# Kernel tuning notes

Measured on AMD Instinct MI355X. Metric: run time of the kernel, lower is better.

Reference implementation:

```python
import jax, jax.numpy as jnp
import numpy as np

EPS = 1e-6        # RMSNorm140 eps
LAM = 0.1         # lambda_: second-order score weight
HAD = 0.05        # hadamard_scale

def _rmsnorm(x, w):
    return x * jax.lax.rsqrt(jnp.mean(x * x, axis=-1, keepdims=True) + EPS) * w

def _rope(x):
    # x: [b, h, s, d]; interleaved-pair rotary embedding (theta=10000)
    b, h, s, d = x.shape
    inv = 1.0 / (10000.0 ** (jnp.arange(0, d, 2, dtype=jnp.float32) / d))
    ang = jnp.arange(s, dtype=jnp.float32)[:, None] * inv[None, :]  # [s, d/2]
    cos, sin = jnp.cos(ang), jnp.sin(ang)
    x1, x2 = x[..., 0::2], x[..., 1::2]
    out = jnp.stack([x1 * cos - x2 * sin, x1 * sin + x2 * cos], axis=-1)
    return out.reshape(b, h, s, d)

def _rotate_half(x):
    d = x.shape[-1] // 2
    return jnp.concatenate([-x[..., d:], x[..., :d]], axis=-1)

def _attn_pass(Q, K, V):
    # scores = (Q@K^T + lam * Q^2 @ (K^2)^T) / sqrt(head_dim)   (second-order amplify)
    scale = 1.0 / jnp.sqrt(jnp.float32(Q.shape[-1]))
    scores = (jnp.einsum('bhsd,bhtd->bhst', Q, K)
              + LAM * jnp.einsum('bhsd,bhtd->bhst', Q * Q, K * K)) * scale
    return jnp.einsum('bhst,bhtd->bhsd', jax.nn.softmax(scores, axis=-1), V)

def _attention(x, wq, wk, wv, wo, gate_w):
    b, s, dim = x.shape
    hd = gate_w.shape[0]
    nh = dim // hd
    def proj(w):  # StickyLinear: x @ W^T, W stored [out, in]
        return (x @ w.T).reshape(b, s, nh, hd).transpose(0, 2, 1, 3)  # [b,h,s,d]
    Q, K, V = proj(wq), proj(wk), proj(wv)
    Q, K = _rope(Q), _rope(K)
    out1 = _attn_pass(Q, K, V)
    # rotated second pass + per-channel sigmoid gate over head_dim
    out2 = _attn_pass(_rotate_half(Q), _rotate_half(K), V)
    g = jax.nn.sigmoid(gate_w)
    out = out1 * (1.0 - g) + out2 * g
    out = out + HAD * out * out  # Hadamard mix (elementwise nonlinearity)
    out = out.transpose(0, 2, 1, 3).reshape(b, s, dim)
    return out @ wo.T

def _ffn(x, w1, w3, w2):
    # SwiGLU: down( silu(gate(x)) * up(x) )
    return (jax.nn.silu(x @ w1.T) * (x @ w3.T)) @ w2.T

def reference(x, norm1_w, norm2_w, wq, wk, wv, wo, gate_w, w1, w3, w2):
    h = x + _attention(_rmsnorm(x, norm1_w), wq, wk, wv, wo, gate_w)
    return h + _ffn(_rmsnorm(h, norm2_w), w1, w3, w2)

def setup_inputs() -> dict:
    B, S, D, NH, DFF = 2, 1024, 2048, 16, 8192
    HD = D // NH
    key = jax.random.key(0)
    ks = jax.random.split(key, 9)
    std = 0.02
    return {
        'x': jax.random.normal(ks[0], (B, S, D), dtype=jnp.float32),
        'norm1_w': jnp.ones((D,), jnp.float32),
        'norm2_w': jnp.ones((D,), jnp.float32),
        'wq': jax.random.normal(ks[1], (D, D), jnp.float32) * std,
        'wk': jax.random.normal(ks[2], (D, D), jnp.float32) * std,
        'wv': jax.random.normal(ks[3], (D, D), jnp.float32) * std,
        'wo': jax.random.normal(ks[4], (D, D), jnp.float32) * std,
        'gate_w': jax.random.normal(ks[5], (HD,), jnp.float32) * 0.01,
        'w1': jax.random.normal(ks[6], (DFF, D), jnp.float32) * std,
        'w3': jax.random.normal(ks[7], (DFF, D), jnp.float32) * std,
        'w2': jax.random.normal(ks[8], (D, DFF), jnp.float32) * std,
    }
```

## Files before the change

kernel.cpp:

```cpp
#include <hip/hip_runtime.h>
#include <hip/hip_bf16.h>

typedef unsigned short u16;
typedef unsigned int u32;
typedef u16 u16x8 __attribute__((ext_vector_type(8)));
typedef float f32x4 __attribute__((ext_vector_type(4)));

__device__ __forceinline__ u16 f2bf(float f) {
  union { float f; u32 u; } v; v.f = f;
  u32 r = v.u + 0x7FFFu + ((v.u >> 16) & 1u);
  return (u16)(r >> 16);
}
__device__ __forceinline__ float bf2f(u16 h) {
  union { u32 u; float f; } v; v.u = ((u32)h) << 16;
  return v.f;
}
__device__ __forceinline__ void mfma_bf16_16x16x32(f32x4& acc, const f32x4& a, const f32x4& b) {
  asm("v_mfma_f32_16x16x32_bf16 %0, %1, %2, %0" : "+v"(acc) : "v"(a), "v"(b));
}
__device__ __forceinline__ void gload_lds16(const void* g, void* l) {
  __builtin_amdgcn_global_load_lds(
      (const __attribute__((address_space(1))) unsigned int*)g,
      (__attribute__((address_space(3))) unsigned int*)l, 16, 0, 0);
}

__global__ __launch_bounds__(256) void cvt_k(const float* __restrict__ src,
                                             u16* __restrict__ dst, int n8) {
  int i = blockIdx.x * 256 + threadIdx.x;
  if (i >= n8) return;
  float4 f0 = *(const float4*)&src[(size_t)i * 8];
  float4 f1 = *(const float4*)&src[(size_t)i * 8 + 4];
  u16x8 o;
  o[0] = f2bf(f0.x); o[1] = f2bf(f0.y); o[2] = f2bf(f0.z); o[3] = f2bf(f0.w);
  o[4] = f2bf(f1.x); o[5] = f2bf(f1.y); o[6] = f2bf(f1.z); o[7] = f2bf(f1.w);
  *(u16x8*)&dst[(size_t)i * 8] = o;
}

__global__ __launch_bounds__(256) void cvt13_k(const float* __restrict__ src,
                                               u16* __restrict__ dst, int half) {
  int r = blockIdx.x;
  int dr = ((r >> 4) << 5) + (r & 15) + (half << 4);
  int t = threadIdx.x;
  const float* s = src + (size_t)r * 2048 + t * 8;
  float4 f0 = *(const float4*)s;
  float4 f1 = *(const float4*)(s + 4);
  u16x8 o;
  o[0] = f2bf(f0.x); o[1] = f2bf(f0.y); o[2] = f2bf(f0.z); o[3] = f2bf(f0.w);
  o[4] = f2bf(f1.x); o[5] = f2bf(f1.y); o[6] = f2bf(f1.z); o[7] = f2bf(f1.w);
  *(u16x8*)&dst[(size_t)dr * 2048 + t * 8] = o;
}

__global__ __launch_bounds__(256) void rmsnorm_k(const float* __restrict__ X,
                                                 const float* __restrict__ W,
                                                 u16* __restrict__ O) {
  const int row = blockIdx.x;
  const int tid = threadIdx.x;
  const float* x = X + (size_t)row * 2048;
  float4 v0 = *(const float4*)&x[tid * 8];
  float4 v1 = *(const float4*)&x[tid * 8 + 4];
  float s = v0.x * v0.x + v0.y * v0.y + v0.z * v0.z + v0.w * v0.w
          + v1.x * v1.x + v1.y * v1.y + v1.z * v1.z + v1.w * v1.w;
  #pragma unroll
  for (int m = 1; m < 64; m <<= 1) s += __shfl_xor(s, m);
  __shared__ float red[4];
  if ((tid & 63) == 0) red[tid >> 6] = s;
  __syncthreads();
  float tot = red[0] + red[1] + red[2] + red[3];
  float r = rsqrtf(tot * (1.0f / 2048.0f) + 1e-6f);
  float4 w0 = *(const float4*)&W[tid * 8];
  float4 w1 = *(const float4*)&W[tid * 8 + 4];
  u16x8 o;
  o[0] = f2bf(v0.x * r * w0.x); o[1] = f2bf(v0.y * r * w0.y);
  o[2] = f2bf(v0.z * r * w0.z); o[3] = f2bf(v0.w * r * w0.w);
  o[4] = f2bf(v1.x * r * w1.x); o[5] = f2bf(v1.y * r * w1.y);
  o[6] = f2bf(v1.z * r * w1.z); o[7] = f2bf(v1.w * r * w1.w);
  *(u16x8*)&O[(size_t)row * 2048 + tid * 8] = o;
}

#define EPI_F32 0
#define EPI_ADDF32 1
#define EPI_SWIGLU 2

template <int EPI>
__global__ __launch_bounds__(256) void gemm_bt(const u16* __restrict__ A,
                                               const u16* __restrict__ B,
                                               float* __restrict__ Cf,
                                               u16* __restrict__ Cb,
                                               const float* __restrict__ R,
                                               int M, int N, int Kt,
                                               int lda, int ldb) {
  __shared__ __align__(16) u16 As[2][128 * 32];
  __shared__ __align__(16) u16 Bs[2][128 * 32];
  const int tid = threadIdx.x;
  const int lane = tid & 63;
  const int w = tid >> 6;
  const int wm = w >> 1, wn = w & 1;
  const int m0 = blockIdx.y * 128, n0 = blockIdx.x * 128;
  const int z = blockIdx.z;
  A += (size_t)z * Kt;
  B += (size_t)z * Kt;
  Cf += (size_t)z * M * N;
  const int r0 = tid >> 2;
  const int c0 = (tid & 3) * 8;
  const int r1 = r0 + 64;
  const int laneM = lane & 15;
  const int laneK = (lane >> 4) * 8;

  f32x4 acc[4][4];
  #pragma unroll
  for (int i = 0; i < 4; i++)
    #pragma unroll
    for (int j = 0; j < 4; j++) acc[i][j] = (f32x4){0.f, 0.f, 0.f, 0.f};

  const u16* Ar0 = &A[(size_t)(m0 + r0) * lda + c0];
  const u16* Ar1 = &A[(size_t)(m0 + r1) * lda + c0];
  const u16* Br0 = &B[(size_t)(n0 + r0) * ldb + c0];
  const u16* Br1 = &B[(size_t)(n0 + r1) * ldb + c0];
  const int lofs0 = r0 * 32 + c0;
  const int lofs1 = r1 * 32 + c0;

  auto stage = [&](int bsel, int kt) {
    gload_lds16(Ar0 + kt, &As[bsel][lofs0]);
    gload_lds16(Ar1 + kt, &As[bsel][lofs1]);
    gload_lds16(Br0 + kt, &Bs[bsel][lofs0]);
    gload_lds16(Br1 + kt, &Bs[bsel][lofs1]);
  };

  stage(0, 0);
  const int nt = Kt >> 5;
  for (int t = 0; t < nt; t++) {
    const int cur = t & 1;
    if (t + 1 < nt) {
      stage(cur ^ 1, (t + 1) << 5);
      asm volatile("s_waitcnt vmcnt(4)" ::: "memory");
    } else {
      asm volatile("s_waitcnt vmcnt(0)" ::: "memory");
    }
    __builtin_amdgcn_s_barrier();
    __builtin_amdgcn_sched_barrier(0);
    f32x4 af[4], bfr[4];
    #pragma unroll
    for (int mi = 0; mi < 4; mi++)
      af[mi] = *(const f32x4*)&As[cur][(wm * 64 + mi * 16 + laneM) * 32 + laneK];
    #pragma unroll
    for (int ni = 0; ni < 4; ni++)
      bfr[ni] = *(const f32x4*)&Bs[cur][(wn * 64 + ni * 16 + laneM) * 32 + laneK];
    #pragma unroll
    for (int mi = 0; mi < 4; mi++)
      #pragma unroll
      for (int ni = 0; ni < 4; ni++)
        mfma_bf16_16x16x32(acc[mi][ni], af[mi], bfr[ni]);
    __builtin_amdgcn_sched_barrier(0);
    __builtin_amdgcn_s_barrier();
  }

  const int rowb = (lane >> 4) * 4;
  const int coll = lane & 15;
  #pragma unroll
  for (int mi = 0; mi < 4; mi++) {
    #pragma unroll
    for (int i = 0; i < 4; i++) {
      int row = m0 + wm * 64 + mi * 16 + rowb + i;
      #pragma unroll
      for (int ni = 0; ni < 4; ni++) {
        int col = n0 + wn * 64 + ni * 16 + coll;
        size_t idx = (size_t)row * N + col;
        float v = acc[mi][ni][i];
        if constexpr (EPI == EPI_F32) Cf[idx] = v;
        else Cf[idx] = v + R[idx];
      }
    }
  }
}

template <int EPI>
__global__ __launch_bounds__(512, 2) void gemm256(const u16* __restrict__ A,
                                                  const u16* __restrict__ B,
                                                  float* __restrict__ Cf,
                                                  u16* __restrict__ Cb,
                                                  int M, int N, int Kt,
                                                  int lda, int ldb) {
  __shared__ __align__(16) char sm[131072];
  const int tid = threadIdx.x;
  const int lane = tid & 63, w = tid >> 6;
  const int wr = w >> 2, wc = w & 3;
  const int laneM = lane & 15, laneG = lane >> 4;
  const int m0 = blockIdx.y * 256, n0 = blockIdx.x * 256;
  const int z = blockIdx.z;
  A += (size_t)z * Kt;
  B += (size_t)z * Kt;
  Cf += (size_t)z * M * N;

  const int srow = tid >> 3;
  const int scb = (tid & 7) * 16;

  f32x4 acc[8][4];
  #pragma unroll
  for (int i = 0; i < 8; i++)
    #pragma unroll
    for (int j = 0; j < 4; j++) acc[i][j] = (f32x4){0.f, 0.f, 0.f, 0.f};

  auto stage = [&](int buf, int ktE, int ht) {
    const int half = ht & 1;
    const bool isA = ht < 2;
    char* base = sm + (isA ? 0 : 65536) + buf * 32768 + half * 16384;
    const u16* src = isA ? A : B;
    const int ld = isA ? lda : ldb;
    const int rb = (isA ? m0 : n0) + half * 128;
    #pragma unroll
    for (int j = 0; j < 2; j++) {
      int row = j * 64 + srow;
      int scol = (scb ^ ((row & 7) << 4)) >> 1;
      gload_lds16(src + (size_t)(rb + row) * ld + ktE + scol,
                  base + j * 8192 + tid * 16);
    }
  };

  const int nkt = Kt >> 6;
  #pragma unroll
  for (int ht = 0; ht < 4; ht++) stage(0, 0, ht);

  const int bHalf = wc >> 1;
  const int bRow0 = (wc & 1) * 64;

  for (int t = 0; t < nkt; t++) {
    const int cb_ = t & 1;
    char* aBase = sm + cb_ * 32768 + wr * 16384;
    char* bBase = sm + 65536 + cb_ * 32768 + bHalf * 16384;
    if (t + 1 < nkt) {
      #pragma unroll
      for (int ht = 0; ht < 4; ht++) stage(cb_ ^ 1, (t + 1) << 6, ht);
      asm volatile("s_waitcnt vmcnt(8)" ::: "memory");
    } else {
      asm volatile("s_waitcnt vmcnt(0)" ::: "memory");
    }
    __builtin_amdgcn_s_barrier();
    #pragma unroll
    for (int q = 0; q < 4; q++) {
      const int mh = q >> 1, nh = q & 1;
      f32x4 af[4][2], bg[2][2];
      #pragma unroll
      for (int mi = 0; mi < 4; mi++)
        #pragma unroll
        for (int ks = 0; ks < 2; ks++) {
          int r = (mh * 4 + mi) * 16 + laneM;
          int cbv = ks * 64 + laneG * 16;
          af[mi][ks] = *(const f32x4*)(aBase + r * 128 + (cbv ^ ((r & 7) << 4)));
        }
      #pragma unroll
      for (int ni = 0; ni < 2; ni++)
        #pragma unroll
        for (int ks = 0; ks < 2; ks++) {
          int r = bRow0 + (nh * 2 + ni) * 16 + laneM;
          int cbv = ks * 64 + laneG * 16;
          bg[ni][ks] = *(const f32x4*)(bBase + r * 128 + (cbv ^ ((r & 7) << 4)));
        }
      if (q > 0) __builtin_amdgcn_s_barrier();
      asm volatile("s_waitcnt lgkmcnt(0)" ::: "memory");
      __builtin_amdgcn_sched_barrier(0);
      __builtin_amdgcn_s_setprio(1);
      #pragma unroll
      for (int mi = 0; mi < 4; mi++)
        #pragma unroll
        for (int ni = 0; ni < 2; ni++)
          #pragma unroll
          for (int ks = 0; ks < 2; ks++)
            mfma_bf16_16x16x32(acc[mh * 4 + mi][nh * 2 + ni], af[mi][ks], bg[ni][ks]);
      __builtin_amdgcn_s_setprio(0);
      __builtin_amdgcn_sched_barrier(0);
      __builtin_amdgcn_s_barrier();
    }
  }

  #pragma unroll
  for (int mi = 0; mi < 8; mi++) {
    #pragma unroll
    for (int i = 0; i < 4; i++) {
      int row = m0 + wr * 128 + mi * 16 + laneG * 4 + i;
      if constexpr (EPI == EPI_SWIGLU) {
        #pragma unroll
        for (int np = 0; np < 2; np++) {
          float g = acc[mi][np * 2][i];
          float u = acc[mi][np * 2 + 1][i];
          float sg = g / (1.0f + __expf(-g));
          int j = (n0 >> 1) + wc * 32 + np * 16 + laneM;
          Cb[(size_t)row * (N >> 1) + j] = f2bf(sg * u);
        }
      } else {
        #pragma unroll
        for (int ni = 0; ni < 4; ni++) {
          int col = n0 + wc * 64 + ni * 16 + laneM;
          Cf[(size_t)row * N + col] = acc[mi][ni][i];
        }
      }
    }
  }
}

__global__ __launch_bounds__(256) void reduce5_k(const float* __restrict__ P,
                                                 const float* __restrict__ H,
                                                 float* __restrict__ out) {
  size_t i = ((size_t)blockIdx.x * 256 + threadIdx.x) * 4;
  const size_t MN = 4194304;
  float4 a = *(const float4*)&P[i];
  float4 b = *(const float4*)&P[MN + i];
  float4 c = *(const float4*)&P[2 * MN + i];
  float4 d = *(const float4*)&P[3 * MN + i];
  float4 h = *(const float4*)&H[i];
  float4 o;
  o.x = a.x + b.x + c.x + d.x + h.x;
  o.y = a.y + b.y + c.y + d.y + h.y;
  o.z = a.z + b.z + c.z + d.z + h.z;
  o.w = a.w + b.w + c.w + d.w + h.w;
  *(float4*)&out[i] = o;
}

__device__ __forceinline__ void rope_row(const float* __restrict__ src,
                                         u16* __restrict__ dst, int s, int q4) {
  float vv[32];
  #pragma unroll
  for (int t = 0; t < 8; t++) {
    float4 f = *(const float4*)&src[t * 4];
    vv[t * 4] = f.x; vv[t * 4 + 1] = f.y; vv[t * 4 + 2] = f.z; vv[t * 4 + 3] = f.w;
  }
  u16 o1[32], o2[32];
  #pragma unroll
  for (int jl = 0; jl < 16; jl++) {
    int j = q4 * 16 + jl;
    float inv = exp2f(-(float)j * 0.20762050593046014f);
    float ang = (float)s * inv;
    float sn, cs;
    __sincosf(ang, &sn, &cs);
    float a = vv[2 * jl], b = vv[2 * jl + 1];
    float r1 = a * cs - b * sn;
    float r2 = a * sn + b * cs;
    o1[2 * jl] = f2bf(r1);
    o1[2 * jl + 1] = f2bf(r2);
    o2[2 * jl] = f2bf(0.31622776601683794f * r1 * r1);
    o2[2 * jl + 1] = f2bf(0.31622776601683794f * r2 * r2);
  }
  #pragma unroll
  for (int t = 0; t < 4; t++) {
    *(u16x8*)&dst[q4 * 32 + t * 8] = *(const u16x8*)&o1[t * 8];
    *(u16x8*)&dst[128 + q4 * 32 + t * 8] = *(const u16x8*)&o2[t * 8];
  }
}

__global__ __launch_bounds__(256) void qkv_post_k(const float* __restrict__ QKVF,
                                                  u16* __restrict__ Qe,
                                                  u16* __restrict__ Ke,
                                                  u16* __restrict__ Vt) {
  const int st = blockIdx.x;
  const int bh = blockIdx.y;
  const int b = bh >> 4, h = bh & 15;
  const int tid = threadIdx.x;
  {
    int r = tid >> 2, q4 = tid & 3;
    int s = st * 64 + r;
    size_t rowin = ((size_t)b * 1024 + s) * 6144 + h * 128 + q4 * 32;
    size_t rowe = ((size_t)bh * 1024 + s) * 256;
    rope_row(QKVF + rowin, Qe + rowe, s, q4);
    rope_row(QKVF + rowin + 2048, Ke + rowe, s, q4);
  }
  __shared__ __align__(16) u16 vts[128 * 72];
  {
    int r = tid >> 2, q4 = tid & 3;
    int s = st * 64 + r;
    const float* src = QKVF + ((size_t)b * 1024 + s) * 6144 + 4096 + h * 128 + q4 * 32;
    #pragma unroll
    for (int k = 0; k < 32; k += 4) {
      float4 f = *(const float4*)&src[k];
      int d = q4 * 32 + k;
      vts[(d + 0) * 72 + r] = f2bf(f.x);
      vts[(d + 1) * 72 + r] = f2bf(f.y);
      vts[(d + 2) * 72 + r] = f2bf(f.z);
      vts[(d + 3) * 72 + r] = f2bf(f.w);
    }
  }
  __syncthreads();
  {
    int d = tid >> 1, sp = (tid & 1) * 32;
    u16* dst = Vt + ((size_t)bh * 128 + d) * 1024 + st * 64 + sp;
    #pragma unroll
    for (int k = 0; k < 32; k += 8)
      *(u16x8*)&dst[k] = *(const u16x8*)&vts[d * 72 + sp + k];
  }
}

__global__ __launch_bounds__(256, 2) void attn_k(const u16* __restrict__ Qe,
                                                 const u16* __restrict__ Ke,
                                                 const u16* __restrict__ Vt,
                                                 u16* __restrict__ AO) {
  const int bh = blockIdx.x;
  const int qt = blockIdx.y;
  const int b = bh >> 4, h = bh & 15;
  const int tid = threadIdx.x;
  const int w = tid >> 6, lane = tid & 63;
  const int laneM = lane & 15, laneG = lane >> 4;

  __shared__ __align__(16) char smem[57344];
  u16* plu = (u16*)(smem + 49152 + w * 2048);

  const char* KeB = (const char*)Ke + (size_t)bh * 524288;
  const char* VtB = (const char*)Vt + (size_t)bh * 262144;

  const size_t qbase = ((size_t)bh * 1024 + qt * 64 + w * 16 + laneM) * 256 + laneG * 8;
  f32x4 qf[8];
  #pragma unroll
  for (int kk = 0; kk < 8; kk++) qf[kk] = *(const f32x4*)&Qe[qbase + kk * 32];

  float m_i[4], l_i[4];
  #pragma unroll
  for (int i = 0; i < 4; i++) { m_i[i] = -1e30f; l_i[i] = 0.f; }
  f32x4 accO[8];
  #pragma unroll
  for (int n = 0; n < 8; n++) accO[n] = (f32x4){0.f, 0.f, 0.f, 0.f};

  u16x8 kreg[4], vreg[2];
  auto loadRegs = [&](int ktn) {
    const char* ks = KeB + (size_t)ktn * 16384;
    #pragma unroll
    for (int j = 0; j < 4; j++) {
      int p = j * 4096 + tid * 16;
      kreg[j] = *(const u16x8*)(ks + p);
    }
    const char* vs = VtB + (size_t)ktn * 64;
    #pragma unroll
    for (int j = 0; j < 2; j++) {
      int p = j * 4096 + tid * 16;
      int r = p >> 6, x = p & 63;
      vreg[j] = *(const u16x8*)(vs + (size_t)r * 2048 + x);
    }
  };
  auto writeLDS = [&](int bsel) {
    char* kd = smem + (bsel ? 16384 : 0);
    #pragma unroll
    for (int j = 0; j < 4; j++) {
      int p = j * 4096 + tid * 16;
      int r = p >> 9, x = p & 511;
      *(u16x8*)(kd + r * 512 + (x ^ ((r & 7) << 4))) = kreg[j];
    }
    char* vd = smem + 32768 + (bsel ? 8192 : 0);
    #pragma unroll
    for (int j = 0; j < 2; j++) {
      int p = j * 4096 + tid * 16;
      int r = p >> 6, x = p & 63;
      *(u16x8*)(vd + r * 64 + (x ^ (((r >> 1) & 3) << 4))) = vreg[j];
    }
  };

  loadRegs(0);
  writeLDS(0);
  int cur = 0;
  const float scale = 0.08838834764831845f;

  for (int kt = 0; kt < 32; kt++) {
    if (kt < 31) loadRegs(kt + 1);
    __syncthreads();
    const char* Kc = smem + (cur ? 16384 : 0);
    const char* Vc = smem + 32768 + (cur ? 8192 : 0);

    f32x4 accS[2];
    #pragma unroll
    for (int n = 0; n < 2; n++) accS[n] = (f32x4){0.f, 0.f, 0.f, 0.f};
    #pragma unroll
    for (int n = 0; n < 2; n++) {
      int r = n * 16 + laneM;
      const char* krow = Kc + r * 512;
      int sw = (r & 7) << 4;
      #pragma unroll
      for (int kk = 0; kk < 8; kk++) {
        f32x4 kf = *(const f32x4*)(krow + ((kk * 64 + laneG * 16) ^ sw));
        mfma_bf16_16x16x32(accS[n], qf[kk], kf);
      }
    }

    float p[2][4], sf[4];
    #pragma unroll
    for (int i = 0; i < 4; i++) {
      float mx = fmaxf(accS[0][i], accS[1][i]) * scale;
      #pragma unroll
      for (int m = 1; m < 16; m <<= 1) mx = fmaxf(mx, __shfl_xor(mx, m));
      float mnew = fmaxf(m_i[i], mx);
      sf[i] = __expf(m_i[i] - mnew);
      m_i[i] = mnew;
      float p0 = __expf(accS[0][i] * scale - mnew);
      float p1 = __expf(accS[1][i] * scale - mnew);
      p[0][i] = p0; p[1][i] = p1;
      float rs = p0 + p1;
      #pragma unroll
      for (int m = 1; m < 16; m <<= 1) rs += __shfl_xor(rs, m);
      l_i[i] = l_i[i] * sf[i] + rs;
    }
    #pragma unroll
    for (int n = 0; n < 8; n++) {
      accO[n][0] *= sf[0]; accO[n][1] *= sf[1];
      accO[n][2] *= sf[2]; accO[n][3] *= sf[3];
    }

    #pragma unroll
    for (int n = 0; n < 2; n++)
      #pragma unroll
      for (int i = 0; i < 4; i++) {
        int row = laneG * 4 + i;
        int col = n * 16 + laneM;
        plu[row * 64 + (col ^ (((row >> 2) & 3) << 4))] = f2bf(p[n][i]);
      }
    f32x4 pa = *(const f32x4*)&plu[laneM * 64 +
                                   ((laneG * 8) ^ (((laneM >> 2) & 3) << 4))];

    #pragma unroll
    for (int n = 0; n < 8; n++) {
      int r = n * 16 + laneM;
      f32x4 vf = *(const f32x4*)(Vc + r * 64 + ((laneG * 16) ^ (((r >> 1) & 3) << 4)));
      mfma_bf16_16x16x32(accO[n], pa, vf);
    }

    if (kt < 31) writeLDS(cur ^ 1);
    cur ^= 1;
  }

  #pragma unroll
  for (int i = 0; i < 4; i++) {
    float inv_l = 1.f / l_i[i];
    int row = b * 1024 + qt * 64 + w * 16 + laneG * 4 + i;
    #pragma unroll
    for (int n = 0; n < 8; n++) {
      float o = accO[n][i] * inv_l;
      o = o + 0.05f * o * o;
      AO[(size_t)row * 2048 + h * 128 + n * 16 + laneM] = f2bf(o);
    }
  }
}

extern "C" void kernel_launch(void* const* d_in, const int* in_sizes, int n_in,
                              void* d_out, int out_size, void* d_ws, size_t ws_size,
                              hipStream_t stream) {
  const float* x   = (const float*)d_in[0];
  const float* n1w = (const float*)d_in[1];
  const float* n2w = (const float*)d_in[2];
  const float* wq  = (const float*)d_in[3];
  const float* wk  = (const float*)d_in[4];
  const float* wv  = (const float*)d_in[5];
  const float* wo  = (const float*)d_in[6];
  const float* w1  = (const float*)d_in[8];
  const float* w3  = (const float*)d_in[9];
  const float* w2  = (const float*)d_in[10];

  char* ws = (char*)d_ws;
  u16* WQKVb = (u16*)(ws + 0);
  u16* WOb   = (u16*)(ws + 25165824);
  u16* W13b  = (u16*)(ws + 33554432);
  u16* W2b   = (u16*)(ws + 100663296);
  u16* XN    = (u16*)(ws + 134217728);
  float* QKVF = (float*)(ws + 142606336);
  u16* U     = (u16*)(ws + 142606336);
  float* P   = (float*)(ws + 176160768);
  u16* QE    = (u16*)(ws + 192937984);
  u16* KE    = (u16*)(ws + 209715200);
  u16* VT    = (u16*)(ws + 226492416);
  u16* AO    = (u16*)(ws + 234881024);
  float* H   = (float*)(ws + 243269632);

  cvt_k<<<2048, 256, 0, stream>>>(wq, WQKVb, 524288);
  cvt_k<<<2048, 256, 0, stream>>>(wk, WQKVb + 4194304, 524288);
  cvt_k<<<2048, 256, 0, stream>>>(wv, WQKVb + 8388608, 524288);
  cvt_k<<<2048, 256, 0, stream>>>(wo, WOb, 524288);
  cvt13_k<<<8192, 256, 0, stream>>>(w1, W13b, 0);
  cvt13_k<<<8192, 256, 0, stream>>>(w3, W13b, 1);
  cvt_k<<<8192, 256, 0, stream>>>(w2, W2b, 2097152);

  rmsnorm_k<<<2048, 256, 0, stream>>>(x, n1w, XN);

  gemm256<EPI_F32><<<dim3(24, 8), 512, 0, stream>>>(
      XN, WQKVb, QKVF, nullptr, 2048, 6144, 2048, 2048, 2048);

  qkv_post_k<<<dim3(16, 32), 256, 0, stream>>>(QKVF, QE, KE, VT);

  attn_k<<<dim3(32, 16), 256, 0, stream>>>(QE, KE, VT, AO);

  gemm_bt<EPI_ADDF32><<<dim3(16, 16), 256, 0, stream>>>(
      AO, WOb, H, nullptr, x, 2048, 2048, 2048, 2048, 2048);

  rmsnorm_k<<<2048, 256, 0, stream>>>(H, n2w, XN);

  gemm256<EPI_SWIGLU><<<dim3(64, 8), 512, 0, stream>>>(
      XN, W13b, nullptr, U, 2048, 16384, 2048, 2048, 2048);

  gemm256<EPI_F32><<<dim3(8, 8, 4), 512, 0, stream>>>(
      U, W2b, P, nullptr, 2048, 2048, 2048, 8192, 8192);

  reduce5_k<<<4096, 256, 0, stream>>>(P, H, (float*)d_out);
}
```

Before: 556.0 us.

## Restructure GEMM k-loop into two halves with split prefetch staging

```diff
diff --git a/kernel.cpp b/kernel.cpp
--- a/kernel.cpp
+++ b/kernel.cpp
@@ -227,49 +227,67 @@
     const int cb_ = t & 1;
     char* aBase = sm + cb_ * 32768 + wr * 16384;
     char* bBase = sm + 65536 + cb_ * 32768 + bHalf * 16384;
-    if (t + 1 < nkt) {
-      #pragma unroll
-      for (int ht = 0; ht < 4; ht++) stage(cb_ ^ 1, (t + 1) << 6, ht);
-      asm volatile("s_waitcnt vmcnt(8)" ::: "memory");
-    } else {
-      asm volatile("s_waitcnt vmcnt(0)" ::: "memory");
-    }
+    const bool pre = (t + 1 < nkt);
+    const int ktE1 = (t + 1) << 6;
+
+    f32x4 af[4][2], bg[4][2];
+
+    if (pre) { stage(cb_ ^ 1, ktE1, 0); stage(cb_ ^ 1, ktE1, 1); }
+    if (pre) asm volatile("s_waitcnt vmcnt(4)" ::: "memory");
+    else     asm volatile("s_waitcnt vmcnt(0)" ::: "memory");
     __builtin_amdgcn_s_barrier();
     #pragma unroll
-    for (int q = 0; q < 4; q++) {
-      const int mh = q >> 1, nh = q & 1;
-      f32x4 af[4][2], bg[2][2];
-      #pragma unroll
-      for (int mi = 0; mi < 4; mi++)
+    for (int ni = 0; ni < 4; ni++)
+      #pragma unroll
+      for (int ks = 0; ks < 2; ks++) {
+        int r = bRow0 + ni * 16 + laneM;
+        int cbv = ks * 64 + laneG * 16;
+        bg[ni][ks] = *(const f32x4*)(bBase + r * 128 + (cbv ^ ((r & 7) << 4)));
+      }
+    #pragma unroll
+    for (int mi = 0; mi < 4; mi++)
+      #pragma unroll
+      for (int ks = 0; ks < 2; ks++) {
+        int r = mi * 16 + laneM;
+        int cbv = ks * 64 + laneG * 16;
+        af[mi][ks] = *(const f32x4*)(aBase + r * 128 + (cbv ^ ((r & 7) << 4)));
+      }
+    asm volatile("s_waitcnt lgkmcnt(0)" ::: "memory");
+    __builtin_amdgcn_sched_barrier(0);
+    __builtin_amdgcn_s_setprio(1);
+    #pragma unroll
+    for (int mi = 0; mi < 4; mi++)
+      #pragma unroll
+      for (int ni = 0; ni < 4; ni++)
         #pragma unroll
-        for (int ks = 0; ks < 2; ks++) {
-          int r = (mh * 4 + mi) * 16 + laneM;
-          int cbv = ks * 64 + laneG * 16;
-          af[mi][ks] = *(const f32x4*)(aBase + r * 128 + (cbv ^ ((r & 7) << 4)));
-        }
-      #pragma unroll
-      for (int ni = 0; ni < 2; ni++)
+        for (int ks = 0; ks < 2; ks++)
+          mfma_bf16_16x16x32(acc[mi][ni], af[mi][ks], bg[ni][ks]);
+    __builtin_amdgcn_s_setprio(0);
+    __builtin_amdgcn_sched_barrier(0);
+
+    if (pre) { stage(cb_ ^ 1, ktE1, 2); stage(cb_ ^ 1, ktE1, 3); }
+    __builtin_amdgcn_s_barrier();
+    #pragma unroll
+    for (int mi = 0; mi < 4; mi++)
+      #pragma unroll
+      for (int ks = 0; ks < 2; ks++) {
+        int r = (4 + mi) * 16 + laneM;
+        int cbv = ks * 64 + laneG * 16;
+        af[mi][ks] = *(const f32x4*)(aBase + r * 128 + (cbv ^ ((r & 7) << 4)));
+      }
+    asm volatile("s_waitcnt lgkmcnt(0)" ::: "memory");
+    __builtin_amdgcn_sched_barrier(0);
+    __builtin_amdgcn_s_setprio(1);
+    #pragma unroll
+    for (int mi = 0; mi < 4; mi++)
+      #pragma unroll
+      for (int ni = 0; ni < 4; ni++)
         #pragma unroll
-        for (int ks = 0; ks < 2; ks++) {
-          int r = bRow0 + (nh * 2 + ni) * 16 + laneM;
-          int cbv = ks * 64 + laneG * 16;
-          bg[ni][ks] = *(const f32x4*)(bBase + r * 128 + (cbv ^ ((r & 7) << 4)));
-        }
-      if (q > 0) __builtin_amdgcn_s_barrier();
-      asm volatile("s_waitcnt lgkmcnt(0)" ::: "memory");
-      __builtin_amdgcn_sched_barrier(0);
-      __builtin_amdgcn_s_setprio(1);
-      #pragma unroll
-      for (int mi = 0; mi < 4; mi++)
-        #pragma unroll
-        for (int ni = 0; ni < 2; ni++)
-          #pragma unroll
-          for (int ks = 0; ks < 2; ks++)
-            mfma_bf16_16x16x32(acc[mh * 4 + mi][nh * 2 + ni], af[mi][ks], bg[ni][ks]);
-      __builtin_amdgcn_s_setprio(0);
-      __builtin_amdgcn_sched_barrier(0);
-      __builtin_amdgcn_s_barrier();
-    }
+        for (int ks = 0; ks < 2; ks++)
+          mfma_bf16_16x16x32(acc[4 + mi][ni], af[mi][ks], bg[ni][ks]);
+    __builtin_amdgcn_s_setprio(0);
+    __builtin_amdgcn_sched_barrier(0);
+    __builtin_amdgcn_s_barrier();
   }
 
   #pragma unroll
```

New measurement: 505.5 us. 9.1% less time.
